# Optimization experiments

Hardware: AMD Instinct MI355X
Metric: run time of the kernel (lower is better)

## Reference

```python
import jax, jax.numpy as jnp
import numpy as np

N_EMBD = 2048
N_HEAD = 16
N_KV_HEAD = 4
HEAD_DIM = N_EMBD // N_HEAD  # 128
N_REP = N_HEAD // N_KV_HEAD  # 4
ROPE_BASE = 1000000.0
B, T = 2, 2048


def _rotate_half(x):
    x1, x2 = jnp.split(x, 2, axis=-1)
    return jnp.concatenate([-x2, x1], axis=-1)


def _rope(q, k, t):
    # q: [b,t,h,d], k: [b,t,kvh,d]; full rotary (partial_rotary_factor=1.0)
    pos = jnp.arange(t, dtype=jnp.float32)
    inv_freq = 1.0 / (ROPE_BASE ** (jnp.arange(0, HEAD_DIM, 2, dtype=jnp.float32) / HEAD_DIM))
    ang = pos[:, None] * inv_freq[None, :]                      # [t, d/2]
    cos = jnp.concatenate([jnp.cos(ang), jnp.cos(ang)], -1)     # [t, d]
    sin = jnp.concatenate([jnp.sin(ang), jnp.sin(ang)], -1)
    cos = cos[None, :, None, :]
    sin = sin[None, :, None, :]
    q = q * cos + _rotate_half(q) * sin
    k = k * cos + _rotate_half(k) * sin
    return q, k


def setup_inputs() -> dict:
    key = jax.random.key(0)
    ks = jax.random.split(key, 9)
    std = 0.02
    proj_std = 0.02 / np.sqrt(2 * 24)
    return {
        "x": jax.random.normal(ks[0], (B, T, N_EMBD), dtype=jnp.float32),
        "Wq": jax.random.normal(ks[1], (N_EMBD, N_HEAD * HEAD_DIM), dtype=jnp.float32) * std,
        "bq": jnp.zeros((N_HEAD * HEAD_DIM,), dtype=jnp.float32),
        "Wk": jax.random.normal(ks[2], (N_EMBD, N_KV_HEAD * HEAD_DIM), dtype=jnp.float32) * std,
        "bk": jnp.zeros((N_KV_HEAD * HEAD_DIM,), dtype=jnp.float32),
        "Wv": jax.random.normal(ks[3], (N_EMBD, N_KV_HEAD * HEAD_DIM), dtype=jnp.float32) * std,
        "bv": jnp.zeros((N_KV_HEAD * HEAD_DIM,), dtype=jnp.float32),
        "Wo": jax.random.normal(ks[4], (N_EMBD, N_EMBD), dtype=jnp.float32) * proj_std,
        "bo": jnp.zeros((N_EMBD,), dtype=jnp.float32),
    }


def reference(x, Wq, bq, Wk, bk, Wv, bv, Wo, bo):
    b, t, _ = x.shape
    q = (x @ Wq + bq).reshape(b, t, N_HEAD, HEAD_DIM)
    k = (x @ Wk + bk).reshape(b, t, N_KV_HEAD, HEAD_DIM)
    v = (x @ Wv + bv).reshape(b, t, N_KV_HEAD, HEAD_DIM)
    q, k = _rope(q, k, t)
    # repeat_kv: expand kv heads by n_rep
    k = jnp.broadcast_to(k[:, :, :, None, :], (b, t, N_KV_HEAD, N_REP, HEAD_DIM)).reshape(b, t, N_HEAD, HEAD_DIM)
    v = jnp.broadcast_to(v[:, :, :, None, :], (b, t, N_KV_HEAD, N_REP, HEAD_DIM)).reshape(b, t, N_HEAD, HEAD_DIM)
    qh = q.transpose(0, 2, 1, 3)  # [b,h,t,d]
    kh = k.transpose(0, 2, 1, 3)
    vh = v.transpose(0, 2, 1, 3)
    causal = jnp.tril(jnp.ones((t, t), dtype=bool))[None, None]  # [1,1,t,t]
    bias = jnp.where(causal, 0.0, -1e9).astype(jnp.float32)
    scores = jnp.einsum('bhtd,bhTd->bhtT', qh, kh) / jnp.sqrt(jnp.float32(HEAD_DIM))
    attn_w = jax.nn.softmax(scores + bias, axis=-1)
    attn_out = jnp.einsum('bhtT,bhTd->bhtd', attn_w, vh)
    attn = attn_out.transpose(0, 2, 1, 3).reshape(b, t, N_EMBD)
    return attn @ Wo + bo
```

## Files before the change

### kernel.cpp

```cpp
#include <hip/hip_runtime.h>

typedef _Float16 f16x8 __attribute__((ext_vector_type(8)));
typedef _Float16 f16x4 __attribute__((ext_vector_type(4)));
typedef float    f32x4 __attribute__((ext_vector_type(4)));

__device__ __forceinline__ void gload16(const void* g, void* l) {
  __builtin_amdgcn_global_load_lds((const __attribute__((address_space(1))) void*)g,
                                   (__attribute__((address_space(3))) void*)l, 16, 0, 0);
}

__global__ __launch_bounds__(256) void cast_f32_f16(const float* __restrict__ src,
                                                    _Float16* __restrict__ dst, int n4) {
  int i = blockIdx.x * 256 + threadIdx.x;
  if (i < n4) {
    f32x4 v = *(const f32x4*)(src + (size_t)i * 4);
    f16x4 o;
    o[0] = (_Float16)v[0]; o[1] = (_Float16)v[1];
    o[2] = (_Float16)v[2]; o[3] = (_Float16)v[3];
    *(f16x4*)(dst + (size_t)i * 4) = o;
  }
}

__global__ __launch_bounds__(256) void wqkvtrans_kernel(const float* __restrict__ Wq,
                                                        const float* __restrict__ Wk,
                                                        const float* __restrict__ Wv,
                                                        _Float16* __restrict__ dst) {
  const int n0 = blockIdx.x * 64, k0 = blockIdx.y * 64;
  const float* src; int N, nb;
  if (n0 < 2048)      { src = Wq; N = 2048; nb = n0; }
  else if (n0 < 2560) { src = Wk; N = 512;  nb = n0 - 2048; }
  else                { src = Wv; N = 512;  nb = n0 - 2560; }
  __shared__ float tile[64][65];
#pragma unroll
  for (int i = 0; i < 16; ++i) {
    int id = i * 256 + threadIdx.x;
    int kk = id >> 6, nn = id & 63;
    tile[kk][nn] = src[(size_t)(k0 + kk) * N + nb + nn];
  }
  __syncthreads();
#pragma unroll
  for (int i = 0; i < 16; ++i) {
    int id = i * 256 + threadIdx.x;
    int nn = id >> 6, kk = id & 63;
    dst[(size_t)(n0 + nn) * 2048 + k0 + kk] = (_Float16)tile[kk][nn];
  }
}

__global__ __launch_bounds__(256) void wtrans_kernel(const float* __restrict__ src,
                                                     _Float16* __restrict__ dst,
                                                     int N, int K, int rowOff, int ldDst) {
  const int n0 = blockIdx.x * 64, k0 = blockIdx.y * 64;
  __shared__ float tile[64][65];
#pragma unroll
  for (int i = 0; i < 16; ++i) {
    int id = i * 256 + threadIdx.x;
    int kk = id >> 6, nn = id & 63;
    tile[kk][nn] = src[(size_t)(k0 + kk) * N + n0 + nn];
  }
  __syncthreads();
#pragma unroll
  for (int i = 0; i < 16; ++i) {
    int id = i * 256 + threadIdx.x;
    int nn = id >> 6, kk = id & 63;
    dst[(size_t)(rowOff + n0 + nn) * ldDst + k0 + kk] = (_Float16)tile[kk][nn];
  }
}

__global__ __launch_bounds__(256) void biaspack_kernel(const float* __restrict__ bq,
                                                       const float* __restrict__ bk,
                                                       const float* __restrict__ bv,
                                                       float* __restrict__ out) {
  int i = blockIdx.x * 256 + threadIdx.x;
  if (i < 3072) out[i] = (i < 2048) ? bq[i] : (i < 2560 ? bk[i - 2048] : bv[i - 2560]);
}

template <bool F16OUT>
__global__ __launch_bounds__(256) void gemm_nt(const _Float16* __restrict__ A,
                                               const _Float16* __restrict__ B,
                                               const float* __restrict__ bias,
                                               void* __restrict__ Cv,
                                               int M, int N, int K) {
  __shared__ __align__(16) _Float16 As[128][64];
  __shared__ __align__(16) _Float16 Bs[128][64];
  const int tid = threadIdx.x;
  const int lane = tid & 63, wave = tid >> 6;
  const int wr = wave >> 1, wc = wave & 1;
  const int r = lane & 15, g = lane >> 4;
  const int rb = blockIdx.y * 128, cb = blockIdx.x * 128;

  const int swz = ((tid & 7) ^ ((tid >> 3) & 7)) * 8;
  const _Float16* aSrc = A + (size_t)(rb + (tid >> 3)) * K + swz;
  const _Float16* bSrc = B + (size_t)(cb + (tid >> 3)) * K + swz;

  f32x4 acc[4][4] = {};

  for (int kt = 0; kt < K; kt += 64) {
    __syncthreads();
#pragma unroll
    for (int p = 0; p < 4; ++p) {
      gload16(aSrc + (size_t)(p * 32) * K + kt, (_Float16*)As + (p * 256 + wave * 64) * 8);
      gload16(bSrc + (size_t)(p * 32) * K + kt, (_Float16*)Bs + (p * 256 + wave * 64) * 8);
    }
    __syncthreads();
#pragma unroll
    for (int kk = 0; kk < 2; ++kk) {
      f16x8 af[4], bf[4];
#pragma unroll
      for (int m = 0; m < 4; ++m) {
        int row = wr * 64 + m * 16 + r;
        af[m] = *(const f16x8*)(&As[row][((kk * 4 + g) ^ (row & 7)) * 8]);
      }
#pragma unroll
      for (int n = 0; n < 4; ++n) {
        int row = wc * 64 + n * 16 + r;
        bf[n] = *(const f16x8*)(&Bs[row][((kk * 4 + g) ^ (row & 7)) * 8]);
      }
#pragma unroll
      for (int m = 0; m < 4; ++m)
#pragma unroll
        for (int n = 0; n < 4; ++n)
          acc[m][n] = __builtin_amdgcn_mfma_f32_16x16x32_f16(af[m], bf[n], acc[m][n], 0, 0, 0);
    }
  }

  float bvals[4];
#pragma unroll
  for (int n = 0; n < 4; ++n) bvals[n] = bias[cb + wc * 64 + n * 16 + r];
#pragma unroll
  for (int m = 0; m < 4; ++m) {
#pragma unroll
    for (int n = 0; n < 4; ++n) {
#pragma unroll
      for (int j = 0; j < 4; ++j) {
        int row = rb + wr * 64 + m * 16 + g * 4 + j;
        int col = cb + wc * 64 + n * 16 + r;
        float v = acc[m][n][j] + bvals[n];
        if (F16OUT)
          ((_Float16*)Cv)[(size_t)row * N + col] = (_Float16)v;
        else
          ((float*)Cv)[(size_t)row * N + col] = v;
      }
    }
  }
}

__global__ __launch_bounds__(256) void rope_kernel(_Float16* __restrict__ QKV) {
  const int tok = blockIdx.x;
  const int t = tok & 2047;
  __shared__ float cs[64], sn[64];
  if (threadIdx.x < 64) {
    int j = threadIdx.x;
    float freq = exp2f((float)(-2 * j) * (19.931568569324174f / 128.0f));
    float ang = (float)t * freq;
    cs[j] = cosf(ang);
    sn[j] = sinf(ang);
  }
  __syncthreads();
  _Float16* base = QKV + (size_t)tok * 3072;
  int idx = threadIdx.x;
  if (idx < 160) {
    int head = idx >> 3, j0 = (idx & 7) * 8;
    int cb = (head < 16) ? head * 128 : 2048 + (head - 16) * 128;
    _Float16* p = base + cb;
    f16x8 a = *(const f16x8*)(p + j0);
    f16x8 b2 = *(const f16x8*)(p + 64 + j0);
    f16x8 oa, ob;
#pragma unroll
    for (int e = 0; e < 8; ++e) {
      float c = cs[j0 + e], s = sn[j0 + e];
      float x1 = (float)a[e], x2 = (float)b2[e];
      oa[e] = (_Float16)(x1 * c - x2 * s);
      ob[e] = (_Float16)(x2 * c + x1 * s);
    }
    *(f16x8*)(p + j0) = oa;
    *(f16x8*)(p + 64 + j0) = ob;
  }
}

__global__ __launch_bounds__(256) void vtrans_kernel(const _Float16* __restrict__ QKV,
                                                     _Float16* __restrict__ Vt) {
  const int bk = blockIdx.z;
  const int t0 = blockIdx.x * 64, d0 = blockIdx.y * 64;
  const int b = bk >> 2, kvh = bk & 3;
  __shared__ _Float16 tile[64][65];
  const _Float16* src = QKV + (size_t)b * 2048 * 3072 + 2560 + kvh * 128;
#pragma unroll
  for (int i = 0; i < 16; ++i) {
    int id = i * 256 + threadIdx.x;
    int tt = id >> 6, dd = id & 63;
    tile[tt][dd] = src[(size_t)(t0 + tt) * 3072 + d0 + dd];
  }
  __syncthreads();
  _Float16* dst = Vt + (size_t)bk * 128 * 2048;
#pragma unroll
  for (int i = 0; i < 16; ++i) {
    int id = i * 256 + threadIdx.x;
    int dd = id >> 6, tt = id & 63;
    dst[(size_t)(d0 + dd) * 2048 + t0 + tt] = tile[tt][dd];
  }
}

__global__ __launch_bounds__(512) void attn_kernel(const _Float16* __restrict__ QKV,
                                                   const _Float16* __restrict__ Vt,
                                                   _Float16* __restrict__ O) {
  const int bid = blockIdx.x;
  const int b = bid >> 8;
  const int ii = bid & 255;
  const int h = ii >> 4;
  const int qtr = ii & 15;
  const int qt = b ? 15 - qtr : qtr;
  const int tid = threadIdx.x;
  const int wave = tid >> 6, lane = tid & 63;
  const int r = lane & 15, g = lane >> 4;
  const int q0 = qt * 128 + wave * 16;
  const int kvh = h >> 2;
  const _Float16* Qb  = QKV + (size_t)b * 2048 * 3072 + h * 128;
  const _Float16* Kb  = QKV + (size_t)b * 2048 * 3072 + 2048 + kvh * 128;
  const _Float16* Vtg = Vt + (size_t)(b * 4 + kvh) * 128 * 2048;

  __shared__ __align__(16) _Float16 Klds[128][128];
  __shared__ __align__(16) _Float16 Vlds[128][128];
  __shared__ __align__(16) _Float16 Plds[8][16][64];

  const int sRow = tid >> 4;
  const int sChunk = ((tid & 15) ^ ((tid >> 4) & 7)) * 8;
  const _Float16* kSrc = Kb  + (size_t)sRow * 3072 + sChunk;
  const _Float16* vSrc = Vtg + (size_t)sRow * 2048 + sChunk;

  f16x8 qf[4];
  {
    const float qsc = 0.08838834764831845f * 1.4426950408889634f;
    const _Float16* qrow = Qb + (size_t)(q0 + r) * 3072 + g * 8;
#pragma unroll
    for (int c = 0; c < 4; ++c) {
      f16x8 v = *(const f16x8*)(qrow + c * 32);
#pragma unroll
      for (int i = 0; i < 8; ++i) v[i] = (_Float16)((float)v[i] * qsc);
      qf[c] = v;
    }
  }

  f32x4 oacc[8] = {};
  float mrun = -1e30f, lrun = 0.f;
  const int kend = qt * 128 + 128;
  const int qlim = q0 + 16;

  for (int kb = 0; kb < kend; kb += 128) {
#pragma unroll
    for (int p = 0; p < 4; ++p) {
      gload16(kSrc + (size_t)(kb + p * 32) * 3072, (_Float16*)Klds + (p * 512 + tid) * 8);
      gload16(vSrc + (size_t)(p * 32) * 2048 + kb, (_Float16*)Vlds + (p * 512 + tid) * 8);
    }
    __syncthreads();
#pragma unroll
    for (int kk2 = 0; kk2 < 128; kk2 += 64) {
      const int kbb = kb + kk2;
      if (kbb >= qlim) break;
      f32x4 sT[4] = {};
      __builtin_amdgcn_s_setprio(1);
#pragma unroll
      for (int c = 0; c < 4; ++c) {
#pragma unroll
        for (int n = 0; n < 4; ++n) {
          f16x8 kf = *(const f16x8*)(&Klds[kk2 + n * 16 + r][(((c * 4 + g) ^ (r & 7)) * 8)]);
          sT[n] = __builtin_amdgcn_mfma_f32_16x16x32_f16(kf, qf[c], sT[n], 0, 0, 0);
        }
      }
      __builtin_amdgcn_s_setprio(0);
      if (kbb + 63 > q0) {
#pragma unroll
        for (int n = 0; n < 4; ++n)
#pragma unroll
          for (int j = 0; j < 4; ++j) {
            int kg = kbb + n * 16 + g * 4 + j;
            if (kg > q0 + r) sT[n][j] = -1e30f;
          }
      }
      float mt = -1e30f;
#pragma unroll
      for (int n = 0; n < 4; ++n)
#pragma unroll
        for (int j = 0; j < 4; ++j) mt = fmaxf(mt, sT[n][j]);
      mt = fmaxf(mt, __shfl_xor(mt, 16));
      mt = fmaxf(mt, __shfl_xor(mt, 32));
      if (__any(mt > mrun)) {
        float mnew = fmaxf(mrun, mt);
        float alpha = exp2f(mrun - mnew);
        lrun *= alpha;
        float al[4];
#pragma unroll
        for (int jj = 0; jj < 4; ++jj) al[jj] = __shfl(alpha, g * 4 + jj);
#pragma unroll
        for (int dt = 0; dt < 8; ++dt)
#pragma unroll
          for (int jj = 0; jj < 4; ++jj) oacc[dt][jj] *= al[jj];
        mrun = mnew;
      }
      float p[4][4];
      float rs = 0.f;
#pragma unroll
      for (int n = 0; n < 4; ++n)
#pragma unroll
        for (int j = 0; j < 4; ++j) {
          p[n][j] = exp2f(sT[n][j] - mrun);
          rs += p[n][j];
        }
      rs += __shfl_xor(rs, 16);
      rs += __shfl_xor(rs, 32);
      lrun += rs;
      asm volatile("" ::: "memory");
#pragma unroll
      for (int n = 0; n < 4; ++n) {
        f16x4 p4;
#pragma unroll
        for (int j = 0; j < 4; ++j) p4[j] = (_Float16)p[n][j];
        int c16s = (2 * n + (g >> 1)) ^ (r & 7);
        *(f16x4*)(&Plds[wave][r][c16s * 8 + (g & 1) * 4]) = p4;
      }
      asm volatile("s_waitcnt lgkmcnt(0)" ::: "memory");
      __builtin_amdgcn_sched_barrier(0);
      f16x8 pa0 = *(const f16x8*)(&Plds[wave][r][((g) ^ (r & 7)) * 8]);
      f16x8 pa1 = *(const f16x8*)(&Plds[wave][r][((4 + g) ^ (r & 7)) * 8]);
      __builtin_amdgcn_s_setprio(1);
#pragma unroll
      for (int dt = 0; dt < 8; ++dt) {
        f16x8 vf0 = *(const f16x8*)(&Vlds[dt * 16 + r][((((kk2 >> 3) + g) ^ (r & 7)) * 8)]);
        oacc[dt] = __builtin_amdgcn_mfma_f32_16x16x32_f16(pa0, vf0, oacc[dt], 0, 0, 0);
        f16x8 vf1 = *(const f16x8*)(&Vlds[dt * 16 + r][((((kk2 >> 3) + 4 + g) ^ (r & 7)) * 8)]);
        oacc[dt] = __builtin_amdgcn_mfma_f32_16x16x32_f16(pa1, vf1, oacc[dt], 0, 0, 0);
      }
      __builtin_amdgcn_s_setprio(0);
    }
    __syncthreads();
  }

  float linv = 1.0f / lrun;
  float li[4];
#pragma unroll
  for (int jj = 0; jj < 4; ++jj) li[jj] = __shfl(linv, g * 4 + jj);
#pragma unroll
  for (int dt = 0; dt < 8; ++dt)
#pragma unroll
    for (int jj = 0; jj < 4; ++jj)
      O[(size_t)(b * 2048 + q0 + g * 4 + jj) * 2048 + h * 128 + dt * 16 + r] =
          (_Float16)(oacc[dt][jj] * li[jj]);
}

extern "C" void kernel_launch(void* const* d_in, const int* in_sizes, int n_in,
                              void* d_out, int out_size, void* d_ws, size_t ws_size,
                              hipStream_t stream) {
  const float* x  = (const float*)d_in[0];
  const float* Wq = (const float*)d_in[1];
  const float* bq = (const float*)d_in[2];
  const float* Wk = (const float*)d_in[3];
  const float* bk = (const float*)d_in[4];
  const float* Wv = (const float*)d_in[5];
  const float* bv = (const float*)d_in[6];
  const float* Wo = (const float*)d_in[7];
  const float* bo = (const float*)d_in[8];
  float* out = (float*)d_out;

  char* ws = (char*)d_ws;
  constexpr size_t QKV_OFF  = 0;
  constexpr size_t VT_OFF   = 25165824;
  constexpr size_t ATTN_OFF = VT_OFF + 4194304;
  constexpr size_t WT_OFF   = ATTN_OFF + 16777216;
  constexpr size_t BIAS_OFF = WT_OFF + 12582912;
  _Float16* QKV  = (_Float16*)(ws + QKV_OFF);
  _Float16* Vt   = (_Float16*)(ws + VT_OFF);
  _Float16* attn = (_Float16*)(ws + ATTN_OFF);
  _Float16* WT   = (_Float16*)(ws + WT_OFF);
  float*    bqkv = (float*)(ws + BIAS_OFF);
  _Float16* xb = (_Float16*)d_out;

  cast_f32_f16<<<8192, 256, 0, stream>>>(x, xb, (2 * 2048 * 2048) / 4);
  wqkvtrans_kernel<<<dim3(48, 32), 256, 0, stream>>>(Wq, Wk, Wv, WT);
  biaspack_kernel<<<12, 256, 0, stream>>>(bq, bk, bv, bqkv);
  gemm_nt<true><<<dim3(3072 / 128, 4096 / 128), 256, 0, stream>>>(xb, WT, bqkv, QKV, 4096, 3072, 2048);
  wtrans_kernel<<<dim3(32, 32), 256, 0, stream>>>(Wo, WT, 2048, 2048, 0, 2048);
  rope_kernel<<<4096, 256, 0, stream>>>(QKV);
  vtrans_kernel<<<dim3(32, 2, 8), 256, 0, stream>>>(QKV, Vt);
  attn_kernel<<<512, 512, 0, stream>>>(QKV, Vt, attn);
  gemm_nt<false><<<dim3(2048 / 128, 4096 / 128), 256, 0, stream>>>(attn, WT, bo, out, 4096, 2048, 2048);
}
```

Measured before the change: 214.8 us.

## Use 256x256 double-buffered MFMA GEMM for QKV projection

```diff
diff --git a/kernel.cpp b/kernel.cpp
--- a/kernel.cpp
+++ b/kernel.cpp
@@ -72,6 +72,123 @@
                                                        float* __restrict__ out) {
   int i = blockIdx.x * 256 + threadIdx.x;
   if (i < 3072) out[i] = (i < 2048) ? bq[i] : (i < 2560 ? bk[i - 2048] : bv[i - 2560]);
+}
+
+__global__ __launch_bounds__(512, 2) void gemm256_nt(const _Float16* __restrict__ A,
+                                                     const _Float16* __restrict__ B,
+                                                     const float* __restrict__ bias,
+                                                     _Float16* __restrict__ C,
+                                                     int M, int N, int K) {
+  __shared__ __align__(16) _Float16 As[2][256 * 64];
+  __shared__ __align__(16) _Float16 Bs[2][256 * 64];
+  const int tid = threadIdx.x;
+  const int lane = tid & 63, wave = tid >> 6;
+  const int wr = wave >> 2, wc = wave & 3;
+  const int r = lane & 15, g = lane >> 4;
+  const int rb = blockIdx.y * 256, cb = blockIdx.x * 256;
+
+  const int swz = ((tid & 7) ^ ((tid >> 3) & 7)) * 8;
+  const _Float16* aSrc = A + (size_t)(rb + (tid >> 3)) * K + swz;
+  const _Float16* bSrc = B + (size_t)(cb + (tid >> 3)) * K + swz;
+
+  f32x4 acc[8][4] = {};
+  f16x8 af[4][2], bf[4][2];
+
+  const int NT = K >> 6;
+
+#pragma unroll
+  for (int i = 0; i < 4; ++i) {
+    gload16(aSrc + (size_t)(i * 64) * K, As[0] + (i * 512 + tid) * 8);
+    gload16(bSrc + (size_t)(i * 64) * K, Bs[0] + (i * 512 + tid) * 8);
+  }
+  asm volatile("s_waitcnt vmcnt(0)" ::: "memory");
+  __builtin_amdgcn_s_barrier();
+
+  auto ldA = [&](_Float16* AsC, int mh) {
+#pragma unroll
+    for (int mi = 0; mi < 4; ++mi)
+#pragma unroll
+      for (int kk = 0; kk < 2; ++kk) {
+        int row = wr * 128 + (mh * 4 + mi) * 16 + r;
+        af[mi][kk] = *(const f16x8*)(AsC + row * 64 + (((kk * 4 + g) ^ (r & 7)) * 8));
+      }
+  };
+  auto ldB = [&](_Float16* BsC, int nh) {
+#pragma unroll
+    for (int ni = 0; ni < 2; ++ni)
+#pragma unroll
+      for (int kk = 0; kk < 2; ++kk) {
+        int row = wc * 64 + (nh * 2 + ni) * 16 + r;
+        bf[nh * 2 + ni][kk] = *(const f16x8*)(BsC + row * 64 + (((kk * 4 + g) ^ (r & 7)) * 8));
+      }
+  };
+  auto mma = [&](int mh, int nh) {
+    __builtin_amdgcn_s_setprio(1);
+#pragma unroll
+    for (int mi = 0; mi < 4; ++mi)
+#pragma unroll
+      for (int ni = 0; ni < 2; ++ni)
+#pragma unroll
+        for (int kk = 0; kk < 2; ++kk)
+          acc[mh * 4 + mi][nh * 2 + ni] = __builtin_amdgcn_mfma_f32_16x16x32_f16(
+              af[mi][kk], bf[nh * 2 + ni][kk], acc[mh * 4 + mi][nh * 2 + ni], 0, 0, 0);
+    __builtin_amdgcn_s_setprio(0);
+  };
+
+  auto ktile = [&](_Float16* AsC, _Float16* BsC, _Float16* AsN, _Float16* BsN,
+                   int ktNext, bool doStage) {
+    ldA(AsC, 0);
+    ldB(BsC, 0);
+    if (doStage) {
+#pragma unroll
+      for (int i = 0; i < 4; ++i)
+        gload16(aSrc + (size_t)ktNext * 64 + (size_t)(i * 64) * K, AsN + (i * 512 + tid) * 8);
+    }
+    __builtin_amdgcn_s_barrier();
+    asm volatile("s_waitcnt lgkmcnt(0)" ::: "memory");
+    __builtin_amdgcn_sched_barrier(0);
+    mma(0, 0);
+    __builtin_amdgcn_s_barrier();
+    ldB(BsC, 1);
+    if (doStage) {
+#pragma unroll
+      for (int i = 0; i < 4; ++i)
+        gload16(bSrc + (size_t)ktNext * 64 + (size_t)(i * 64) * K, BsN + (i * 512 + tid) * 8);
+    }
+    __builtin_amdgcn_s_barrier();
+    asm volatile("s_waitcnt lgkmcnt(0)" ::: "memory");
+    __builtin_amdgcn_sched_barrier(0);
+    mma(0, 1);
+    __builtin_amdgcn_s_barrier();
+    ldA(AsC, 1);
+    __builtin_amdgcn_s_barrier();
+    asm volatile("s_waitcnt lgkmcnt(0)" ::: "memory");
+    __builtin_amdgcn_sched_barrier(0);
+    mma(1, 0);
+    __builtin_amdgcn_s_barrier();
+    mma(1, 1);
+    asm volatile("s_waitcnt vmcnt(0)" ::: "memory");
+    __builtin_amdgcn_s_barrier();
+  };
+
+  for (int kt = 0; kt < NT; kt += 2) {
+    ktile(As[0], Bs[0], As[1], Bs[1], kt + 1, kt + 1 < NT);
+    ktile(As[1], Bs[1], As[0], Bs[0], kt + 2, kt + 2 < NT);
+  }
+
+  float bvals[4];
+#pragma unroll
+  for (int n = 0; n < 4; ++n) bvals[n] = bias[cb + wc * 64 + n * 16 + r];
+#pragma unroll
+  for (int m = 0; m < 8; ++m)
+#pragma unroll
+    for (int n = 0; n < 4; ++n)
+#pragma unroll
+      for (int j = 0; j < 4; ++j) {
+        int row = rb + wr * 128 + m * 16 + g * 4 + j;
+        int col = cb + wc * 64 + n * 16 + r;
+        C[(size_t)row * N + col] = (_Float16)(acc[m][n][j] + bvals[n]);
+      }
 }
 
 template <bool F16OUT>
@@ -376,7 +493,7 @@
   cast_f32_f16<<<8192, 256, 0, stream>>>(x, xb, (2 * 2048 * 2048) / 4);
   wqkvtrans_kernel<<<dim3(48, 32), 256, 0, stream>>>(Wq, Wk, Wv, WT);
   biaspack_kernel<<<12, 256, 0, stream>>>(bq, bk, bv, bqkv);
-  gemm_nt<true><<<dim3(3072 / 128, 4096 / 128), 256, 0, stream>>>(xb, WT, bqkv, QKV, 4096, 3072, 2048);
+  gemm256_nt<<<dim3(3072 / 256, 4096 / 256), 512, 0, stream>>>(xb, WT, bqkv, QKV, 4096, 3072, 2048);
   wtrans_kernel<<<dim3(32, 32), 256, 0, stream>>>(Wo, WT, 2048, 2048, 0, 2048);
   rope_kernel<<<4096, 256, 0, stream>>>(QKV);
   vtrans_kernel<<<dim3(32, 2, 8), 256, 0, stream>>>(QKV, Vt);
```

After: 212.8 us. Within noise of the previous version (-0.9%).
